# Kernel optimization log

Measured on AMD Instinct MI355X. Metric: run time of the kernel, lower is better.

## Reference

```python
import jax, jax.numpy as jnp
import numpy as np

V, E, H = 32000, 512, 512
B, T = 32, 512


def setup_inputs() -> dict:
    key = jax.random.key(0)
    ks = jax.random.split(key, 8)
    s_e = 1.0 / np.sqrt(E)
    s_h = 1.0 / np.sqrt(H)
    return {
        "x": jax.random.randint(ks[0], (B, T), 0, V),
        "hidden_f": jnp.zeros((B, H), jnp.float32),
        "hidden_b": jnp.zeros((B, H), jnp.float32),
        "emb": jax.random.normal(ks[1], (V, E), jnp.float32) * 0.02,
        "Wf": jax.random.normal(ks[2], (E, H), jnp.float32) * s_e,
        "Uf": jax.random.normal(ks[3], (H, H), jnp.float32) * s_h,
        "bf": jnp.zeros((H,), jnp.float32),
        "Wb": jax.random.normal(ks[4], (E, H), jnp.float32) * s_e,
        "Ub": jax.random.normal(ks[5], (H, H), jnp.float32) * s_h,
        "bb": jnp.zeros((H,), jnp.float32),
    }


def _rnn_scan(xproj_tbh, h0, U):
    # xproj_tbh: [T,B,H] precomputed x_t @ W + b; vanilla RNN: h_t = tanh(xp_t + h_{t-1} @ U)
    def step(h, xp):
        h = jnp.tanh(xp + h @ U)
        return h, h
    h_last, hs = jax.lax.scan(step, h0, xproj_tbh)
    return hs, h_last  # hs: [T,B,H]


def reference(x, hidden_f, hidden_b, emb, Wf, Uf, bf, Wb, Ub, bb):
    e = emb[x]  # [B,T,E] embedding lookup
    # precompute input projections once (hoists the big GEMM out of the scan)
    xf = jnp.einsum("bte,eh->tbh", e, Wf) + bf  # [T,B,H]
    xb = jnp.einsum("bte,eh->tbh", e, Wb) + bb
    # forward direction
    hs_f, state_f = _rnn_scan(xf, hidden_f, Uf)
    # backward direction: process reversed sequence, then flip outputs back
    hs_b_rev, state_b = _rnn_scan(xb[::-1], hidden_b, Ub)
    hs_b = hs_b_rev[::-1]
    # concat merge -> [B,T,2H]
    output = jnp.concatenate([hs_f, hs_b], axis=-1).transpose(1, 0, 2)
    return output, state_f, state_b
```

## Files before the change

kernel.cpp:

```cpp
#include <hip/hip_runtime.h>

typedef unsigned short u16;
typedef unsigned int u32;
typedef __attribute__((ext_vector_type(8))) _Float16 half8;
typedef __attribute__((ext_vector_type(4))) float f32x4;
typedef __attribute__((ext_vector_type(4))) u32 u32x4;

#define B_ 32
#define T_ 512
#define OFF_WP   ((size_t)0)
#define OFF_UFP  ((size_t)1 << 20)
#define OFF_UBP  (((size_t)1 << 20) + ((size_t)512 << 10))
#define OFF_APK  ((size_t)2 << 20)
#define OFF_XP   ((size_t)18 << 20)
#define OUT_ELEMS ((size_t)B_ * T_ * 1024)

__device__ __forceinline__ u16 f2h(float f) {
  _Float16 h = (_Float16)f; u16 r; __builtin_memcpy(&r, &h, 2); return r;
}
__device__ __forceinline__ float h2f(u16 b) {
  _Float16 h; __builtin_memcpy(&h, &b, 2); return (float)h;
}
__device__ __forceinline__ u32 pkh(float a, float b) {
  return (u32)f2h(a) | ((u32)f2h(b) << 16);
}
__device__ __forceinline__ float tanh_fast(float s) {
  float e2 = __expf(2.f * s);
  return 1.f - 2.f * __builtin_amdgcn_rcpf(e2 + 1.f);
}

__global__ void pack_WU(const float* __restrict__ Wf, const float* __restrict__ Wb,
                        const float* __restrict__ Uf, const float* __restrict__ Ub,
                        u16* __restrict__ Wp, u16* __restrict__ Ufp, u16* __restrict__ Ubp) {
  int tid = blockIdx.x * 256 + threadIdx.x;
  const float* src; u16* dst; int NT, k, n0;
  if (tid < 65536) {
    k = tid >> 7; n0 = (tid & 127) * 8;
    src = (n0 < 512) ? (Wf + (size_t)k * 512 + n0) : (Wb + (size_t)k * 512 + (n0 - 512));
    dst = Wp; NT = 64;
  } else if (tid < 98304) {
    int q = tid - 65536; k = q >> 6; n0 = (q & 63) * 8;
    src = Uf + (size_t)k * 512 + n0; dst = Ufp; NT = 32;
  } else {
    int q = tid - 98304; k = q >> 6; n0 = (q & 63) * 8;
    src = Ub + (size_t)k * 512 + n0; dst = Ubp; NT = 32;
  }
  float4 v0 = *(const float4*)src;
  float4 v1 = *(const float4*)(src + 4);
  float v[8] = {v0.x, v0.y, v0.z, v0.w, v1.x, v1.y, v1.z, v1.w};
  int kt = k >> 5, lhi = (k >> 3) & 3, jj = k & 7;
#pragma unroll
  for (int j = 0; j < 8; ++j) {
    int n = n0 + j, nt = n >> 4, llo = n & 15;
    dst[((size_t)(kt * NT + nt) * 64 + lhi * 16 + llo) * 8 + jj] = f2h(v[j]);
  }
}

__global__ void gather_pack_A(const int* __restrict__ x, const float* __restrict__ emb,
                              u16* __restrict__ Apk) {
  int tid = blockIdx.x * 256 + threadIdx.x;
  int l = tid & 63, kt = (tid >> 6) & 15, mt = tid >> 10;
  int m = mt * 16 + (l & 15);
  int tok = x[m];
  int k0 = kt * 32 + ((l >> 4) << 3);
  const float* src = emb + (size_t)tok * 512 + k0;
  float4 v0 = *(const float4*)src;
  float4 v1 = *(const float4*)(src + 4);
  uint4 o;
  o.x = pkh(v0.x, v0.y); o.y = pkh(v0.z, v0.w);
  o.z = pkh(v1.x, v1.y); o.w = pkh(v1.z, v1.w);
  *(uint4*)(Apk + (size_t)tid * 8) = o;
}

__launch_bounds__(256)
__global__ void gemm_xp(const u16* __restrict__ Apk, const u16* __restrict__ Wp,
                        const float* __restrict__ bf, const float* __restrict__ bb,
                        u16* __restrict__ xp) {
  int bid = blockIdx.x;
  int bm = bid >> 3, bn = bid & 7;
  int tid = threadIdx.x, l = tid & 63, wid = tid >> 6;
  int wm = wid >> 1, wn = wid & 1;
  int mt0 = bm * 8 + wm * 4;
  int nt0 = bn * 8 + wn * 4;
  const half8* Ap = (const half8*)Apk;
  const half8* Bp = (const half8*)Wp;
  f32x4 acc[4][4] = {};
#pragma unroll 2
  for (int kt = 0; kt < 16; ++kt) {
    half8 a[4], b[4];
#pragma unroll
    for (int i = 0; i < 4; ++i) a[i] = Ap[(size_t)((mt0 + i) * 16 + kt) * 64 + l];
#pragma unroll
    for (int j = 0; j < 4; ++j) b[j] = Bp[(size_t)(kt * 64 + nt0 + j) * 64 + l];
#pragma unroll
    for (int i = 0; i < 4; ++i)
#pragma unroll
      for (int j = 0; j < 4; ++j)
        acc[i][j] = __builtin_amdgcn_mfma_f32_16x16x32_f16(a[i], b[j], acc[i][j], 0, 0, 0);
  }
  int lr = l >> 4, lc = l & 15;
#pragma unroll
  for (int j = 0; j < 4; ++j) {
    int col = (nt0 + j) * 16 + lc;
    int dirw = col >> 9, h = col & 511;
    float bias = dirw ? bb[h] : bf[h];
    int sw = h >> 6, snt = (h >> 4) & 3, slc = h & 15;
#pragma unroll
    for (int i2 = 0; i2 < 4; ++i2) {
#pragma unroll
      for (int r = 0; r < 4; ++r) {
        int m = (mt0 + i2) * 16 + lr * 4 + r;
        int b = m >> 9, t = m & 511;
        int halfb = (b >> 4) & 1, rb = b & 15;
        int slr = rb >> 2, sre = rb & 3;
        int stid = sw * 64 + slr * 16 + slc;
        int e = snt * 4 + sre;
        xp[(((size_t)(t * 2 + dirw) * 2 + halfb) * 512 + stid) * 16 + e] =
            f2h(acc[i2][j][r] + bias);
      }
    }
  }
}

__launch_bounds__(512, 2)
__global__ void rnn_scan3(const u16* __restrict__ xp, const u16* __restrict__ Ufp,
                          const u16* __restrict__ Ubp, const float* __restrict__ hidden_f,
                          const float* __restrict__ hidden_b, float* __restrict__ out,
                          float* __restrict__ state_f, float* __restrict__ state_b) {
  __shared__ u16 hl[16 * 512];
  __shared__ u16 uls[128 * 512];
  int tid = threadIdx.x, l = tid & 63, w = tid >> 6;
  int dir = blockIdx.x >> 1, half = blockIdx.x & 1;
  int b0 = half * 16;
  int lr = l >> 4, lc = l & 15;
  const u16* Up = dir ? Ubp : Ufp;
  const float* hid = dir ? hidden_b : hidden_f;
  float* st = dir ? state_b : state_f;

  half8 ub[4][8];
#pragma unroll
  for (int nt = 0; nt < 4; ++nt)
#pragma unroll
    for (int kt = 0; kt < 8; ++kt) {
      ub[nt][kt] = *(const half8*)(Up + ((size_t)(kt * 32 + (w * 4 + nt)) * 64 + l) * 8);
      asm volatile("" : "+v"(ub[nt][kt]));
    }
  half8 sr[4][4];
#pragma unroll
  for (int nt = 0; nt < 4; ++nt)
#pragma unroll
    for (int j = 0; j < 4; ++j) {
      sr[nt][j] = *(const half8*)(Up + ((size_t)((12 + j) * 32 + (w * 4 + nt)) * 64 + l) * 8);
      asm volatile("" : "+v"(sr[nt][j]));
    }
  for (int idx = tid; idx < 128 * 64; idx += 512) {
    int fid = idx >> 6, lane = idx & 63;
    int ntg = fid >> 2, ku = (fid & 3) + 8;
    *(uint4*)(&uls[(size_t)fid * 512 + lane * 8]) =
        *(const uint4*)(Up + ((size_t)(ku * 32 + ntg) * 64 + lane) * 8);
  }
  for (int e = tid; e < 16 * 512; e += 512) {
    int row = e >> 9, col = e & 511;
    hl[(row * 512 + col) ^ ((row & 7) << 3)] = f2h(hid[(size_t)(b0 + row) * 512 + col]);
  }
  __syncthreads();

  int arow = lc;
  int acolb = lr * 8;
  int asw = (arow & 7) << 3;

  for (int i = 0; i < 512; ++i) {
    int t = dir ? (511 - i) : i;
    const u32* xsrc = (const u32*)(xp + (((size_t)(t * 2 + dir) * 2 + half) * 512 + tid) * 16);
    u32x4 xv0 = __builtin_nontemporal_load((const u32x4*)xsrc);
    u32x4 xv1 = __builtin_nontemporal_load(((const u32x4*)xsrc) + 1);

    f32x4 acc[4] = {};
#pragma unroll
    for (int kt = 0; kt < 16; ++kt) {
      half8 a = *(const half8*)(&hl[(arow * 512 + kt * 32 + acolb) ^ asw]);
#pragma unroll
      for (int nt = 0; nt < 4; ++nt) {
        half8 b;
        if (kt < 8)       b = ub[nt][kt];
        else if (kt < 12) b = *(const half8*)(&uls[(size_t)((w * 4 + nt) * 4 + (kt - 8)) * 512 + l * 8]);
        else              b = sr[nt][kt - 12];
        acc[nt] = __builtin_amdgcn_mfma_f32_16x16x32_f16(a, b, acc[nt], 0, 0, 0);
      }
    }
    u16 xe[16];
    __builtin_memcpy(xe, &xv0, 16);
    __builtin_memcpy(xe + 8, &xv1, 16);
    u32 hvp[8];
#pragma unroll
    for (int nt = 0; nt < 4; ++nt) {
      int col = w * 64 + nt * 16 + lc;
      float hv[4];
#pragma unroll
      for (int r = 0; r < 4; ++r) {
        int e = nt * 4 + r;
        float sv = acc[nt][r] + h2f(xe[e]);
        hv[r] = tanh_fast(sv);
        int row = b0 + lr * 4 + r;
        __builtin_nontemporal_store(hv[r],
            out + ((size_t)row * 512 + t) * 1024 + dir * 512 + col);
        if (i == 511) st[(size_t)row * 512 + col] = hv[r];
      }
      hvp[nt * 2]     = pkh(hv[0], hv[1]);
      hvp[nt * 2 + 1] = pkh(hv[2], hv[3]);
    }
    __syncthreads();
    if (i < 511) {
#pragma unroll
      for (int nt = 0; nt < 4; ++nt) {
        int col = w * 64 + nt * 16 + lc;
#pragma unroll
        for (int r = 0; r < 4; ++r) {
          int row = lr * 4 + r;
          u16 hb = (u16)(hvp[nt * 2 + (r >> 1)] >> ((r & 1) * 16));
          hl[(row * 512 + col) ^ ((row & 7) << 3)] = hb;
        }
      }
      __syncthreads();
    }
  }
}

extern "C" void kernel_launch(void* const* d_in, const int* in_sizes, int n_in,
                              void* d_out, int out_size, void* d_ws, size_t ws_size,
                              hipStream_t stream) {
  const int* x = (const int*)d_in[0];
  const float* hidden_f = (const float*)d_in[1];
  const float* hidden_b = (const float*)d_in[2];
  const float* emb = (const float*)d_in[3];
  const float* Wf = (const float*)d_in[4];
  const float* Uf = (const float*)d_in[5];
  const float* bf = (const float*)d_in[6];
  const float* Wb = (const float*)d_in[7];
  const float* Ub = (const float*)d_in[8];
  const float* bb = (const float*)d_in[9];
  float* out = (float*)d_out;

  char* ws = (char*)d_ws;
  u16* Wp  = (u16*)(ws + OFF_WP);
  u16* Ufp = (u16*)(ws + OFF_UFP);
  u16* Ubp = (u16*)(ws + OFF_UBP);
  u16* Apk = (u16*)(ws + OFF_APK);
  u16* xpw = (u16*)(ws + OFF_XP);

  pack_WU<<<512, 256, 0, stream>>>(Wf, Wb, Uf, Ub, Wp, Ufp, Ubp);
  gather_pack_A<<<4096, 256, 0, stream>>>(x, emb, Apk);
  gemm_xp<<<1024, 256, 0, stream>>>(Apk, Wp, bf, bb, xpw);
  rnn_scan3<<<4, 512, 0, stream>>>(xpw, Ufp, Ubp, hidden_f, hidden_b,
                                   out, out + OUT_ELEMS,
                                   out + OUT_ELEMS + (size_t)B_ * 512);
}
```

Baseline: 1.595 ms.

## Halve scan block to 4 waves, each owning 128 columns with AGPR-resident weights

The recurrent scan kernel now uses 256 threads (4 waves) per block instead of 512. Each wave computes 8 column tiles instead of 4 and keeps 12 of the 16 K-slices of U in registers, 4 in VGPRs and 8 pinned to AGPRs. Only the last 4 K-slices are staged in LDS. The xproj layout written by the GEMM is changed to match the new per-thread ownership of 32 elements. The aim is cheaper per-step block barriers with fewer waves and more register-resident weight reuse, at the cost of twice the MFMA work per wave, which lengthens the serial critical path of each step.

```diff
diff --git a/kernel.cpp b/kernel.cpp
--- a/kernel.cpp
+++ b/kernel.cpp
@@ -104,7 +104,7 @@
     int col = (nt0 + j) * 16 + lc;
     int dirw = col >> 9, h = col & 511;
     float bias = dirw ? bb[h] : bf[h];
-    int sw = h >> 6, snt = (h >> 4) & 3, slc = h & 15;
+    int sw2 = h >> 7, snt = (h >> 4) & 7, slc = h & 15;
 #pragma unroll
     for (int i2 = 0; i2 < 4; ++i2) {
 #pragma unroll
@@ -113,20 +113,21 @@
         int b = m >> 9, t = m & 511;
         int halfb = (b >> 4) & 1, rb = b & 15;
         int slr = rb >> 2, sre = rb & 3;
-        int stid = sw * 64 + slr * 16 + slc;
+        int stid = sw2 * 64 + slr * 16 + slc;
         int e = snt * 4 + sre;
-        xp[(((size_t)(t * 2 + dirw) * 2 + halfb) * 512 + stid) * 16 + e] =
+        xp[(((size_t)(t * 2 + dirw) * 2 + halfb) * 256 + stid) * 32 + e] =
             f2h(acc[i2][j][r] + bias);
       }
     }
   }
 }
 
-__launch_bounds__(512, 2)
-__global__ void rnn_scan3(const u16* __restrict__ xp, const u16* __restrict__ Ufp,
-                          const u16* __restrict__ Ubp, const float* __restrict__ hidden_f,
-                          const float* __restrict__ hidden_b, float* __restrict__ out,
-                          float* __restrict__ state_f, float* __restrict__ state_b) {
+__global__ void __launch_bounds__(256)
+__attribute__((amdgpu_waves_per_eu(1)))
+rnn_scan4(const u16* __restrict__ xp, const u16* __restrict__ Ufp,
+          const u16* __restrict__ Ubp, const float* __restrict__ hidden_f,
+          const float* __restrict__ hidden_b, float* __restrict__ out,
+          float* __restrict__ state_f, float* __restrict__ state_b) {
   __shared__ u16 hl[16 * 512];
   __shared__ u16 uls[128 * 512];
   int tid = threadIdx.x, l = tid & 63, w = tid >> 6;
@@ -137,29 +138,29 @@
   const float* hid = dir ? hidden_b : hidden_f;
   float* st = dir ? state_b : state_f;
 
-  half8 ub[4][8];
-#pragma unroll
-  for (int nt = 0; nt < 4; ++nt)
+  half8 uv[8][4];
+#pragma unroll
+  for (int nt = 0; nt < 8; ++nt)
+#pragma unroll
+    for (int kt = 0; kt < 4; ++kt) {
+      uv[nt][kt] = *(const half8*)(Up + ((size_t)(kt * 32 + (w * 8 + nt)) * 64 + l) * 8);
+      asm volatile("" : "+v"(uv[nt][kt]));
+    }
+  half8 ua[8][8];
+#pragma unroll
+  for (int nt = 0; nt < 8; ++nt)
 #pragma unroll
     for (int kt = 0; kt < 8; ++kt) {
-      ub[nt][kt] = *(const half8*)(Up + ((size_t)(kt * 32 + (w * 4 + nt)) * 64 + l) * 8);
-      asm volatile("" : "+v"(ub[nt][kt]));
-    }
-  half8 sr[4][4];
-#pragma unroll
-  for (int nt = 0; nt < 4; ++nt)
-#pragma unroll
-    for (int j = 0; j < 4; ++j) {
-      sr[nt][j] = *(const half8*)(Up + ((size_t)((12 + j) * 32 + (w * 4 + nt)) * 64 + l) * 8);
-      asm volatile("" : "+v"(sr[nt][j]));
-    }
-  for (int idx = tid; idx < 128 * 64; idx += 512) {
+      ua[nt][kt] = *(const half8*)(Up + ((size_t)((kt + 4) * 32 + (w * 8 + nt)) * 64 + l) * 8);
+      asm volatile("" : "+a"(ua[nt][kt]));
+    }
+  for (int idx = tid; idx < 128 * 64; idx += 256) {
     int fid = idx >> 6, lane = idx & 63;
-    int ntg = fid >> 2, ku = (fid & 3) + 8;
+    int ntg = fid >> 2, ku = (fid & 3) + 12;
     *(uint4*)(&uls[(size_t)fid * 512 + lane * 8]) =
         *(const uint4*)(Up + ((size_t)(ku * 32 + ntg) * 64 + lane) * 8);
   }
-  for (int e = tid; e < 16 * 512; e += 512) {
+  for (int e = tid; e < 16 * 512; e += 256) {
     int row = e >> 9, col = e & 511;
     hl[(row * 512 + col) ^ ((row & 7) << 3)] = f2h(hid[(size_t)(b0 + row) * 512 + col]);
   }
@@ -171,35 +172,38 @@
 
   for (int i = 0; i < 512; ++i) {
     int t = dir ? (511 - i) : i;
-    const u32* xsrc = (const u32*)(xp + (((size_t)(t * 2 + dir) * 2 + half) * 512 + tid) * 16);
-    u32x4 xv0 = __builtin_nontemporal_load((const u32x4*)xsrc);
-    u32x4 xv1 = __builtin_nontemporal_load(((const u32x4*)xsrc) + 1);
-
-    f32x4 acc[4] = {};
+    const u32x4* xs = (const u32x4*)(xp + (((size_t)(t * 2 + dir) * 2 + half) * 256 + tid) * 32);
+    u32x4 xv0 = __builtin_nontemporal_load(xs);
+    u32x4 xv1 = __builtin_nontemporal_load(xs + 1);
+    u32x4 xv2 = __builtin_nontemporal_load(xs + 2);
+    u32x4 xv3 = __builtin_nontemporal_load(xs + 3);
+
+    f32x4 acc[8] = {};
 #pragma unroll
     for (int kt = 0; kt < 16; ++kt) {
       half8 a = *(const half8*)(&hl[(arow * 512 + kt * 32 + acolb) ^ asw]);
 #pragma unroll
-      for (int nt = 0; nt < 4; ++nt) {
+      for (int nt = 0; nt < 8; ++nt) {
         half8 b;
-        if (kt < 8)       b = ub[nt][kt];
-        else if (kt < 12) b = *(const half8*)(&uls[(size_t)((w * 4 + nt) * 4 + (kt - 8)) * 512 + l * 8]);
-        else              b = sr[nt][kt - 12];
+        if (kt < 4)       b = uv[nt][kt];
+        else if (kt < 12) b = ua[nt][kt - 4];
+        else              b = *(const half8*)(&uls[(size_t)((w * 8 + nt) * 4 + (kt - 12)) * 512 + l * 8]);
         acc[nt] = __builtin_amdgcn_mfma_f32_16x16x32_f16(a, b, acc[nt], 0, 0, 0);
       }
     }
-    u16 xe[16];
-    __builtin_memcpy(xe, &xv0, 16);
-    __builtin_memcpy(xe + 8, &xv1, 16);
-    u32 hvp[8];
-#pragma unroll
-    for (int nt = 0; nt < 4; ++nt) {
-      int col = w * 64 + nt * 16 + lc;
+    u16 xe[32];
+    __builtin_memcpy(xe,      &xv0, 16);
+    __builtin_memcpy(xe + 8,  &xv1, 16);
+    __builtin_memcpy(xe + 16, &xv2, 16);
+    __builtin_memcpy(xe + 24, &xv3, 16);
+    u32 hvp[16];
+#pragma unroll
+    for (int nt = 0; nt < 8; ++nt) {
+      int col = w * 128 + nt * 16 + lc;
       float hv[4];
 #pragma unroll
       for (int r = 0; r < 4; ++r) {
-        int e = nt * 4 + r;
-        float sv = acc[nt][r] + h2f(xe[e]);
+        float sv = acc[nt][r] + h2f(xe[nt * 4 + r]);
         hv[r] = tanh_fast(sv);
         int row = b0 + lr * 4 + r;
         __builtin_nontemporal_store(hv[r],
@@ -212,8 +216,8 @@
     __syncthreads();
     if (i < 511) {
 #pragma unroll
-      for (int nt = 0; nt < 4; ++nt) {
-        int col = w * 64 + nt * 16 + lc;
+      for (int nt = 0; nt < 8; ++nt) {
+        int col = w * 128 + nt * 16 + lc;
 #pragma unroll
         for (int r = 0; r < 4; ++r) {
           int row = lr * 4 + r;
@@ -251,7 +255,7 @@
   pack_WU<<<512, 256, 0, stream>>>(Wf, Wb, Uf, Ub, Wp, Ufp, Ubp);
   gather_pack_A<<<4096, 256, 0, stream>>>(x, emb, Apk);
   gemm_xp<<<1024, 256, 0, stream>>>(Apk, Wp, bf, bb, xpw);
-  rnn_scan3<<<4, 512, 0, stream>>>(xpw, Ufp, Ubp, hidden_f, hidden_b,
+  rnn_scan4<<<4, 256, 0, stream>>>(xpw, Ufp, Ubp, hidden_f, hidden_b,
                                    out, out + OUT_ELEMS,
                                    out + OUT_ELEMS + (size_t)B_ * 512);
 }
```

Result: slower. 2.126 ms (+33.4%).
